# Performance work log

Measured on AMD Instinct MI355X. Metric: run time of the kernel, lower is better.

## Reference

```python
import jax, jax.numpy as jnp
import numpy as np
import math

D_IN, D_MODEL, N_HEADS, DIM_HEAD, NB_FEAT, N_CLASSES = 24, 512, 8, 64, 266, 10
FF_DIM = 4 * D_MODEL  # performer-pytorch FeedForward mult=4
LN_EPS = 1e-5
B, N = 16, 2048


def gaussian_orthogonal(key, nb_rows, nb_cols):
    # FAVOR+ gaussian orthogonal random matrix (scaling=0: chi-distributed row norms)
    n_blocks = nb_rows // nb_cols + 1
    keys = jax.random.split(key, n_blocks + 1)
    blocks = []
    for i in range(n_blocks):
        q, _ = jnp.linalg.qr(jax.random.normal(keys[i], (nb_cols, nb_cols)))
        blocks.append(q.T)
    mat = jnp.concatenate(blocks, axis=0)[:nb_rows]
    multiplier = jnp.linalg.norm(jax.random.normal(keys[-1], (nb_rows, nb_cols)), axis=1)
    return multiplier[:, None] * mat


def layer_norm(x, g, b):
    mu = jnp.mean(x, axis=-1, keepdims=True)
    var = jnp.var(x, axis=-1, keepdims=True)
    return (x - mu) * jax.lax.rsqrt(var + LN_EPS) * g + b


def softmax_kernel(data, proj, is_query, eps=1e-4):
    # FAVOR+ positive random features approximating the softmax kernel
    data_norm = data.shape[-1] ** -0.25
    ratio = proj.shape[0] ** -0.5
    dd = jnp.einsum('bhnd,fd->bhnf', data * data_norm, proj)  # [B,H,N,F]
    diag = 0.5 * jnp.sum(data * data, axis=-1, keepdims=True) * (data_norm ** 2)
    if is_query:
        m = jax.lax.stop_gradient(jnp.max(dd, axis=-1, keepdims=True))
    else:
        m = jax.lax.stop_gradient(jnp.max(dd))
    return ratio * (jnp.exp(dd - diag - m) + eps)


def setup_inputs() -> dict:
    key = jax.random.key(0)
    ks = jax.random.split(key, 24)

    def linw(k, fi, fo):
        bnd = 1.0 / math.sqrt(fi)
        return jax.random.uniform(k, (fi, fo), minval=-bnd, maxval=bnd, dtype=jnp.float32)

    def linb(k, fi, fo):
        bnd = 1.0 / math.sqrt(fi)
        return jax.random.uniform(k, (fo,), minval=-bnd, maxval=bnd, dtype=jnp.float32)

    return {
        'x': jax.random.normal(ks[0], (B, N, D_IN), dtype=jnp.float32),
        'enc_w': linw(ks[1], D_IN, D_MODEL), 'enc_b': linb(ks[2], D_IN, D_MODEL),
        'ln1_g': jnp.ones((D_MODEL,), jnp.float32), 'ln1_b': jnp.zeros((D_MODEL,), jnp.float32),
        'wq': linw(ks[3], D_MODEL, D_MODEL), 'bq': linb(ks[4], D_MODEL, D_MODEL),
        'wk': linw(ks[5], D_MODEL, D_MODEL), 'bk': linb(ks[6], D_MODEL, D_MODEL),
        'wv': linw(ks[7], D_MODEL, D_MODEL), 'bv': linb(ks[8], D_MODEL, D_MODEL),
        'wo': linw(ks[9], D_MODEL, D_MODEL), 'bo': linb(ks[10], D_MODEL, D_MODEL),
        'proj': gaussian_orthogonal(ks[11], NB_FEAT, DIM_HEAD).astype(jnp.float32),
        'ln2_g': jnp.ones((D_MODEL,), jnp.float32), 'ln2_b': jnp.zeros((D_MODEL,), jnp.float32),
        'ff_w1': linw(ks[12], D_MODEL, FF_DIM), 'ff_b1': linb(ks[13], D_MODEL, FF_DIM),
        'ff_w2': linw(ks[14], FF_DIM, D_MODEL), 'ff_b2': linb(ks[15], FF_DIM, D_MODEL),
        'mlp_w1': linw(ks[16], D_MODEL, D_MODEL), 'mlp_b1': linb(ks[17], D_MODEL, D_MODEL),
        'mlp_w2': linw(ks[18], D_MODEL, N_CLASSES), 'mlp_b2': linb(ks[19], D_MODEL, N_CLASSES),
    }


def reference(x, enc_w, enc_b, ln1_g, ln1_b, wq, bq, wk, bk, wv, bv, wo, bo, proj,
              ln2_g, ln2_b, ff_w1, ff_b1, ff_w2, ff_b2, mlp_w1, mlp_b1, mlp_w2, mlp_b2):
    b, n, _ = x.shape
    h = (x @ enc_w + enc_b) * math.sqrt(D_MODEL)  # [B,N,D]

    # --- Performer layer: PreLN + FAVOR+ self-attention ---
    y = layer_norm(h, ln1_g, ln1_b)
    split = lambda t: t.reshape(b, n, N_HEADS, DIM_HEAD).transpose(0, 2, 1, 3)  # [B,H,N,Dh]
    q = split(y @ wq + bq)
    k = split(y @ wk + bk)
    v = split(y @ wv + bv)
    qp = softmax_kernel(q, proj, is_query=True)   # [B,H,N,F]
    kp = softmax_kernel(k, proj, is_query=False)  # [B,H,N,F]
    # non-causal linear attention
    k_sum = kp.sum(axis=2)                                   # [B,H,F]
    d_inv = 1.0 / jnp.einsum('bhnf,bhf->bhn', qp, k_sum)     # [B,H,N]
    ctx = jnp.einsum('bhnf,bhnd->bhfd', kp, v)               # [B,H,F,Dh]
    attn = jnp.einsum('bhnf,bhfd,bhn->bhnd', qp, ctx, d_inv)
    attn = attn.transpose(0, 2, 1, 3).reshape(b, n, D_MODEL)
    h = h + attn @ wo + bo

    y = layer_norm(h, ln2_g, ln2_b)
    h = h + jax.nn.gelu(y @ ff_w1 + ff_b1, approximate=False) @ ff_w2 + ff_b2

    # --- max pool over sequence + MLP head ---
    p = jnp.max(h, axis=1)  # [B,D]
    return jax.nn.relu(p @ mlp_w1 + mlp_b1) @ mlp_w2 + mlp_b2  # [B,n_classes]
```

## Files before the change

### kernel.cpp

```cpp
#include <hip/hip_runtime.h>
#include <math.h>

typedef unsigned short u16;
typedef __bf16 bf16x8 __attribute__((ext_vector_type(8)));
typedef float f32x4 __attribute__((ext_vector_type(4)));
typedef u16 u16x8 __attribute__((ext_vector_type(8)));

#define DEVI static __device__ __forceinline__

#define NB 16
#define SEQ 2048
#define DM 512
#define DH 64
#define NF 266
#define NFP 288
#define FFD 2048
#define ROWS (NB*SEQ)
#define SQRT_DM 22.62741699796952f
#define DATA_NORM 0.3535533905932738f
#define RATIO 0.0613139073f
#define KEPS 1e-4f

DEVI u16 f2b(float f){
  union{float f; unsigned u;} c; c.f=f;
  unsigned r = c.u + 0x7FFFu + ((c.u>>16)&1u);
  return (u16)(r>>16);
}
DEVI float b2f(u16 v){
  union{unsigned u; float f;} c; c.u = ((unsigned)v)<<16; return c.f;
}
DEVI unsigned cvtpk(float a, float b){
  unsigned r;
  asm("v_cvt_pk_bf16_f32 %0, %1, %2" : "=v"(r) : "v"(a), "v"(b));
  return r;
}

DEVI f32x4 MFMA(bf16x8 a, bf16x8 b, f32x4 c){
  return __builtin_amdgcn_mfma_f32_16x16x32_bf16(a,b,c,0,0,0);
}

DEVI void async16(void* lds, const void* g){
  __builtin_amdgcn_global_load_lds(
      (const __attribute__((address_space(1))) unsigned*)g,
      (__attribute__((address_space(3))) unsigned*)lds, 16, 0, 0);
}

DEVI void atomicMaxF(float* a, float v){
  if (v >= 0.f) atomicMax((int*)a, __float_as_int(v));
  else          atomicMin((unsigned*)a, (unsigned)__float_as_int(v));
}

DEVI bf16x8 ldb8(const u16* p){ return *(const bf16x8*)p; }

DEVI float erf_fast(float u){
  float au = fabsf(u);
  float tt = __builtin_amdgcn_rcpf(1.f + 0.3275911f*au);
  float poly = tt*(0.254829592f + tt*(-0.284496736f + tt*(1.421413741f + tt*(-1.453152027f + tt*1.061405429f))));
  float er = 1.f - poly*__expf(-u*u);
  return copysignf(er, u);
}

template<int EPI>
__launch_bounds__(256,2)
__global__ void gemm_tn(const u16* __restrict__ A, int lda,
                        const u16* __restrict__ Bt, int ldb,
                        const float* __restrict__ bias,
                        float* __restrict__ resid,
                        u16* __restrict__ Cb,
                        int N, int K)
{
  __shared__ u16 As[2][128*32];
  __shared__ u16 Bs[2][128*32];
  const int t = threadIdx.x;
  const int ntn = N >> 7;
  int bid = blockIdx.x;
  const int nwg = gridDim.x;
  if ((nwg & 7) == 0){ int qq = nwg >> 3; bid = (bid & 7)*qq + (bid >> 3); }
  const int bm = bid / ntn, bn = bid % ntn;
  const int w = t>>6, l = t&63, lr = l&15, lg = l>>4;
  const int wr = (w>>1)*64, wc = (w&1)*64;
  const u16* ga = A  + (size_t)(bm*128 + (t>>2))*lda + (t&3)*8;
  const u16* gb = Bt + (size_t)(bn*128 + (t>>2))*ldb + (t&3)*8;
  const int nk = K >> 5;
  f32x4 acc[4][4];
  #pragma unroll
  for (int i=0;i<4;i++)
    #pragma unroll
    for (int j=0;j<4;j++) acc[i][j]=(f32x4){0.f,0.f,0.f,0.f};

  async16(&As[0][t*8], ga);
  async16(&As[0][64*32 + t*8], ga + (size_t)64*lda);
  async16(&Bs[0][t*8], gb);
  async16(&Bs[0][64*32 + t*8], gb + (size_t)64*ldb);

  for (int kt=0; kt<nk; ++kt){
    __syncthreads();
    if (kt+1 < nk){
      const u16* ga2 = ga + (kt+1)*32;
      const u16* gb2 = gb + (kt+1)*32;
      int nbuf = (kt+1)&1;
      async16(&As[nbuf][t*8], ga2);
      async16(&As[nbuf][64*32 + t*8], ga2 + (size_t)64*lda);
      async16(&Bs[nbuf][t*8], gb2);
      async16(&Bs[nbuf][64*32 + t*8], gb2 + (size_t)64*ldb);
    }
    const u16* as = As[kt&1];
    const u16* bs = Bs[kt&1];
    bf16x8 af[4], bff[4];
    #pragma unroll
    for (int i=0;i<4;i++) af[i]  = ldb8(&as[(wr + i*16 + lr)*32 + lg*8]);
    #pragma unroll
    for (int i=0;i<4;i++) bff[i] = ldb8(&bs[(wc + i*16 + lr)*32 + lg*8]);
    #pragma unroll
    for (int i=0;i<4;i++)
      #pragma unroll
      for (int j=0;j<4;j++)
        acc[i][j] = MFMA(af[i], bff[j], acc[i][j]);
  }

  const int r0 = bm*128 + wr + lg*4;
  const int c0 = bn*128 + wc + lr;
  #pragma unroll
  for (int i=0;i<4;i++){
    #pragma unroll
    for (int j=0;j<4;j++){
      #pragma unroll
      for (int q=0;q<4;q++){
        int r = r0 + i*16 + q;
        int c = c0 + j*16;
        float v = acc[i][j][q] + bias[c];
        if (EPI==2) v = 0.5f*v*(1.f + erf_fast(v*0.70710678f));
        size_t idx = (size_t)r*N + c;
        if (EPI==3) resid[idx] = resid[idx] + v;
        else        Cb[idx] = f2b(v);
      }
    }
  }
}

__launch_bounds__(256)
__global__ void k_prep(const float* __restrict__ wq, const float* __restrict__ wk,
                       const float* __restrict__ wv, const float* __restrict__ wo,
                       const float* __restrict__ ffw1, const float* __restrict__ ffw2,
                       const float* __restrict__ proj, const float* __restrict__ bk,
                       const float* __restrict__ bv,
                       u16* __restrict__ wqT, u16* __restrict__ wkvT, u16* __restrict__ woT,
                       u16* __restrict__ f1T, u16* __restrict__ f2T, u16* __restrict__ pjn,
                       float* __restrict__ kvb, float* __restrict__ pbuf)
{
  int bid = blockIdx.x, t = threadIdx.x;
  if (bid < 3072){
    const float* src; u16* dst; int R, C, tile;
    if      (bid < 256){ src=wq;  dst=wqT;          R=512; C=512;  tile=bid; }
    else if (bid < 512){ src=wk;  dst=wkvT;         R=512; C=512;  tile=bid-256; }
    else if (bid < 768){ src=wv;  dst=wkvT+262144;  R=512; C=512;  tile=bid-512; }
    else if (bid <1024){ src=wo;  dst=woT;          R=512; C=512;  tile=bid-768; }
    else if (bid <2048){ src=ffw1;dst=f1T;          R=512; C=2048; tile=bid-1024; }
    else               { src=ffw2;dst=f2T;          R=2048;C=512;  tile=bid-2048; }
    int ntc = C>>5;
    int tr = tile/ntc, tc = tile%ntc;
    __shared__ float tl[32][33];
    int r = t>>5, c = t&31;
    #pragma unroll
    for (int it=0; it<4; ++it)
      tl[r+it*8][c] = src[(size_t)(tr*32 + r + it*8)*C + tc*32 + c];
    __syncthreads();
    #pragma unroll
    for (int it=0; it<4; ++it)
      dst[(size_t)(tc*32 + r + it*8)*R + tr*32 + c] = f2b(tl[c][r+it*8]);
    return;
  }
  int i = (bid-3072)*256 + t;
  if (i < NFP*DH){ int f=i>>6, d=i&63; pjn[i] = f2b(f<NF ? proj[(size_t)f*64+d]*DATA_NORM : 0.f); return; }
  i -= NFP*DH;
  if (i < 1024){ kvb[i] = (i<512)? bk[i] : bv[i-512]; return; }
  i -= 1024;
  if (i < NB*DM){ pbuf[i] = -INFINITY; return; }
}

__global__ void k_signal(float* out, float v){
  if (threadIdx.x==0 && blockIdx.x==0) out[0] = v;
}

__launch_bounds__(256)
__global__ void k_encode_ln(const float* __restrict__ x, const float* __restrict__ ew,
                            const float* __restrict__ eb, const float* __restrict__ lgw,
                            const float* __restrict__ lbw, float* __restrict__ h,
                            u16* __restrict__ y)
{
  int w = threadIdx.x>>6, l = threadIdx.x&63;
  int row = blockIdx.x*4 + w;
  const float* xr = x + (size_t)row*24;
  float xv[24];
  #pragma unroll
  for (int k=0;k<24;k++) xv[k] = xr[k];
  int c0 = l*8;
  float a[8] = {0,0,0,0,0,0,0,0};
  #pragma unroll
  for (int k=0;k<24;k++){
    const float* wp = ew + (size_t)k*DM + c0;
    #pragma unroll
    for (int c=0;c<8;c++) a[c] += xv[k]*wp[c];
  }
  float s=0.f, s2=0.f;
  #pragma unroll
  for (int c=0;c<8;c++){
    a[c] = (a[c] + eb[c0+c]) * SQRT_DM;
    s += a[c]; s2 += a[c]*a[c];
  }
  #pragma unroll
  for (int m=1;m<64;m<<=1){ s += __shfl_xor(s,m); s2 += __shfl_xor(s2,m); }
  float mu = s*(1.f/DM);
  float rs = rsqrtf(s2*(1.f/DM) - mu*mu + 1e-5f);
  float* hr = h + (size_t)row*DM + c0;
  u16 yv[8];
  #pragma unroll
  for (int c=0;c<8;c++){
    hr[c] = a[c];
    yv[c] = f2b((a[c]-mu)*rs*lgw[c0+c] + lbw[c0+c]);
  }
  *(uint4*)(y + (size_t)row*DM + c0) = *(const uint4*)yv;
}

__launch_bounds__(256)
__global__ void k_ln(const float* __restrict__ h, const float* __restrict__ lgw,
                     const float* __restrict__ lbw, u16* __restrict__ y)
{
  int w = threadIdx.x>>6, l = threadIdx.x&63;
  int row = blockIdx.x*4 + w;
  int c0 = l*8;
  const float* hr = h + (size_t)row*DM + c0;
  float a[8];
  *(float4*)&a[0] = *(const float4*)hr;
  *(float4*)&a[4] = *(const float4*)(hr+4);
  float s=0.f, s2=0.f;
  #pragma unroll
  for (int c=0;c<8;c++){ s += a[c]; s2 += a[c]*a[c]; }
  #pragma unroll
  for (int m=1;m<64;m<<=1){ s += __shfl_xor(s,m); s2 += __shfl_xor(s2,m); }
  float mu = s*(1.f/DM);
  float rs = rsqrtf(s2*(1.f/DM) - mu*mu + 1e-5f);
  u16 yv[8];
  #pragma unroll
  for (int c=0;c<8;c++) yv[c] = f2b((a[c]-mu)*rs*lgw[c0+c] + lbw[c0+c]);
  *(uint4*)(y + (size_t)row*DM + c0) = *(const uint4*)yv;
}

__launch_bounds__(256,1)
__global__ void k_kmax(const u16* __restrict__ kv, const u16* __restrict__ pjn,
                       float* __restrict__ mkpart)
{
  __shared__ float red[4];
  int t = threadIdx.x, w = t>>6, l = t&63, lr = l&15, lg = l>>4;
  int bh = blockIdx.x>>3, tile = blockIdx.x&7;
  int b = bh>>3, hd = bh&7;
  int row0 = tile*256 + w*64;
  bf16x8 pf0[17], pf1[17];
  #pragma unroll
  for (int f=0; f<17; ++f){
    const u16* pb = pjn + (f*16 + lr)*64 + lg*8;
    pf0[f] = ldb8(pb); pf1[f] = ldb8(pb+32);
  }
  bf16x8 a0[4], a1[4];
  #pragma unroll
  for (int it=0; it<4; ++it){
    const u16* kb = kv + ((size_t)(b*SEQ + row0 + it*16 + lr)*1024 + hd*64 + lg*8);
    a0[it] = ldb8(kb); a1[it] = ldb8(kb+32);
  }
  float vmax = -3e38f;
  #pragma unroll
  for (int it=0; it<4; ++it){
    #pragma unroll
    for (int f=0; f<17; ++f){
      f32x4 z = (f32x4){0.f,0.f,0.f,0.f};
      z = MFMA(a0[it], pf0[f], z);
      z = MFMA(a1[it], pf1[f], z);
      if (f*16 + lr < NF){
        #pragma unroll
        for (int j=0;j<4;j++) vmax = fmaxf(vmax, z[j]);
      }
    }
  }
  #pragma unroll
  for (int m=1;m<64;m<<=1) vmax = fmaxf(vmax, __shfl_xor(vmax,m));
  if (l==0) red[w] = vmax;
  __syncthreads();
  if (t==0) mkpart[blockIdx.x] = fmaxf(fmaxf(red[0],red[1]), fmaxf(red[2],red[3]));
}

__global__ void k_kmax_red(const float* __restrict__ mkpart, float* __restrict__ mk){
  __shared__ float red[4];
  int t = threadIdx.x, w = t>>6, l = t&63;
  float v = fmaxf(fmaxf(mkpart[t], mkpart[t+256]), fmaxf(mkpart[t+512], mkpart[t+768]));
  #pragma unroll
  for (int m=1;m<64;m<<=1) v = fmaxf(v, __shfl_xor(v,m));
  if (l==0) red[w] = v;
  __syncthreads();
  if (t==0) mk[0] = fmaxf(fmaxf(red[0],red[1]), fmaxf(red[2],red[3]));
}

__launch_bounds__(256,2)
__global__ void k_kpctx(const u16* __restrict__ kv, const u16* __restrict__ pjn,
                        const float* __restrict__ mkp,
                        u16* __restrict__ ctxp, float* __restrict__ ksump)
{
  __shared__ u16 pjs[272*64];
  __shared__ u16 vT[DH*32];
  __shared__ u16 kpT[NFP*32];
  __shared__ float dbuf[4][16];
  int t = threadIdx.x, w = t>>6, l = t&63, lr = l&15, lg = l>>4;
  int bh = blockIdx.x>>2, seg = blockIdx.x&3;
  int b = bh>>3, hd = bh&7;
  int mw = w>>1, fh = (w&1)*9;
  float mk = *mkp;

  for (int i=t; i<2176; i+=256){
    int row = i>>3, cin = i&7;
    *(uint4*)&pjs[row*64 + ((cin ^ (row&7))<<3)] = ((const uint4*)pjn)[i];
  }

  f32x4 ctxa[18];
  #pragma unroll
  for (int f=0;f<18;f++) ctxa[f]=(f32x4){0.f,0.f,0.f,0.f};
  float ksa[9];
  #pragma unroll
  for (int i=0;i<9;i++) ksa[i]=0.f;

  for (int ch=0; ch<16; ++ch){
    int n0 = seg*512 + ch*32;
    __syncthreads();
    {
      int nl = t>>3, d0 = (t&7)*8;
      const u16* vsrc = kv + ((size_t)(b*SEQ + n0 + nl)*1024 + 512 + hd*64 + d0);
      uint4 vv = *(const uint4*)vsrc;
      const u16* vp = (const u16*)&vv;
      #pragma unroll
      for (int i=0;i<8;i++){
        int row = d0+i;
        vT[row*32 + (((nl>>3) ^ ((row>>1)&3))<<3) + (nl&7)] = vp[i];
      }
    }
    const u16* kb = kv + ((size_t)(b*SEQ + n0 + mw*16 + lr)*1024 + hd*64 + lg*8);
    bf16x8 a0 = ldb8(kb), a1 = ldb8(kb+32);
    float sq = 0.f;
    #pragma unroll
    for (int i=0;i<8;i++){ float u0=(float)a0[i], u1=(float)a1[i]; sq += u0*u0 + u1*u1; }
    sq += __shfl_xor(sq,16); sq += __shfl_xor(sq,32);
    if (l<16) dbuf[w][l] = sq*0.0625f;
    #pragma unroll
    for (int ff=0; ff<9; ++ff){
      int f = fh + ff;
      f32x4 z = (f32x4){0.f,0.f,0.f,0.f};
      if (f < 17){
        int row = f*16 + lr;
        const u16* pb0 = pjs + row*64 + ((lg ^ (lr&7))<<3);
        const u16* pb1 = pjs + row*64 + (((lg+4) ^ (lr&7))<<3);
        z = MFMA(a0, ldb8(pb0), z);
        z = MFMA(a1, ldb8(pb1), z);
      }
      float kp0 = RATIO*(__expf(z[0] - dbuf[w][lg*4+0] - mk) + KEPS);
      float kp1 = RATIO*(__expf(z[1] - dbuf[w][lg*4+1] - mk) + KEPS);
      float kp2 = RATIO*(__expf(z[2] - dbuf[w][lg*4+2] - mk) + KEPS);
      float kp3 = RATIO*(__expf(z[3] - dbuf[w][lg*4+3] - mk) + KEPS);
      ksa[ff] += kp0 + kp1 + kp2 + kp3;
      ushort4 kw;
      kw.x = f2b(kp0); kw.y = f2b(kp1); kw.z = f2b(kp2); kw.w = f2b(kp3);
      int row = f*16 + lr;
      int wch = (mw*2 + (lg>>1)) ^ ((row>>1)&3);
      *(ushort4*)&kpT[row*32 + (wch<<3) + ((lg&1)<<2)] = kw;
    }
    __syncthreads();
    int rr = w*16 + lr;
    bf16x8 av = ldb8(&vT[rr*32 + ((lg ^ ((rr>>1)&3))<<3)]);
    #pragma unroll
    for (int f=0;f<18;f++){
      int row = f*16 + lr;
      ctxa[f] = MFMA(av, ldb8(&kpT[row*32 + ((lg ^ ((row>>1)&3))<<3)]), ctxa[f]);
    }
  }

  __syncthreads();
  {
    float* tb = (w&1) ? (float*)pjs : (float*)kpT;
    u16* dstq = ctxp + (((size_t)seg*128 + bh)*DH + w*16)*NFP;
    #pragma unroll
    for (int r=0; r<2; ++r){
      if ((w>>1) == r){
        #pragma unroll
        for (int f=0;f<18;f++)
          #pragma unroll
          for (int j=0;j<4;j++)
            tb[(lg*4+j)*NFP + f*16 + lr] = ctxa[f][j];
        asm volatile("s_waitcnt lgkmcnt(0)" ::: "memory");
        #pragma unroll
        for (int k=0;k<9;k++){
          int c = k*64 + l;
          f32x4 v0 = *(const f32x4*)(tb + c*8);
          f32x4 v1 = *(const f32x4*)(tb + c*8 + 4);
          u16x8 o;
          o[0]=f2b(v0[0]); o[1]=f2b(v0[1]); o[2]=f2b(v0[2]); o[3]=f2b(v0[3]);
          o[4]=f2b(v1[0]); o[5]=f2b(v1[1]); o[6]=f2b(v1[2]); o[7]=f2b(v1[3]);
          *(u16x8*)(dstq + c*8) = o;
        }
      }
      __syncthreads();
    }
  }
  #pragma unroll
  for (int ff=0;ff<9;ff++){
    float v = ksa[ff];
    v += __shfl_xor(v,16); v += __shfl_xor(v,32);
    if (l<16) ksump[((size_t)seg*128 + bh)*NFP + (fh+ff)*16 + l] = v;
  }
}

__global__ void k_reduce(const u16* __restrict__ ctxp, const float* __restrict__ ksump,
                         u16* __restrict__ ctxb, float* __restrict__ ksum)
{
  const size_t CT = (size_t)128*DH*NFP;
  const size_t KT = (size_t)128*NFP;
  size_t i = (size_t)blockIdx.x*256 + threadIdx.x;
  if (i < CT){
    float s = b2f(ctxp[i]) + b2f(ctxp[i+CT]) + b2f(ctxp[i+2*CT]) + b2f(ctxp[i+3*CT]);
    ctxb[i] = f2b(s);
  } else if (i < CT + KT){
    size_t j = i - CT;
    ksum[j] = ksump[j] + ksump[j+KT] + ksump[j+2*KT] + ksump[j+3*KT];
  }
}

__launch_bounds__(256,3)
__global__ void k_qp_attn(const u16* __restrict__ q, const u16* __restrict__ pjn,
                          const u16* __restrict__ ctxb, const float* __restrict__ ksum,
                          u16* __restrict__ attn)
{
  __shared__ u16 ob[4][16*72];
  int t = threadIdx.x, w = t>>6, l = t&63, lr = l&15, lg = l>>4;
  int bh = blockIdx.x>>5, tile = blockIdx.x&31;
  int b = bh>>3, hd = bh&7;
  int n0 = tile*64;
  const u16* qb = q + ((size_t)(b*SEQ + n0 + w*16 + lr)*DM + hd*64 + lg*8);
  bf16x8 a0 = ldb8(qb), a1 = ldb8(qb+32);
  float sq = 0.f;
  #pragma unroll
  for (int i=0;i<8;i++){ float u0=(float)a0[i], u1=(float)a1[i]; sq += u0*u0 + u1*u1; }
  sq += __shfl_xor(sq,16); sq += __shfl_xor(sq,32);
  float dg = sq*0.0625f;

  float mj = -3e38f;
  #pragma unroll
  for (int ft=0; ft<17; ++ft){
    const u16* pb = pjn + (ft*16 + lr)*64 + lg*8;
    f32x4 z = (f32x4){0.f,0.f,0.f,0.f};
    z = MFMA(ldb8(pb), a0, z);
    z = MFMA(ldb8(pb+32), a1, z);
    if (ft < 16){
      #pragma unroll
      for (int j=0;j<4;j++) mj = fmaxf(mj, z[j]);
    } else {
      #pragma unroll
      for (int j=0;j<4;j++) if (lg*4+j < 10) mj = fmaxf(mj, z[j]);
    }
  }
  mj = fmaxf(mj, __shfl_xor(mj,16));
  mj = fmaxf(mj, __shfl_xor(mj,32));

  int s0 = ((lg&1)<<5) + lr;
  int s1 = s0 + 16;
  bool hi = (l >= 32);
  f32x4 oacc[4];
  #pragma unroll
  for (int d=0;d<4;d++) oacc[d]=(f32x4){0.f,0.f,0.f,0.f};
  const u16* cbase = ctxb + (size_t)bh*DH*NFP;
  const float* ksb = ksum + (size_t)bh*NFP;
  float den = 0.f;
  #pragma unroll
  for (int fp=0; fp<9; ++fp){
    int te = 2*fp, to = te+1;
    f32x4 z0 = (f32x4){0.f,0.f,0.f,0.f};
    f32x4 z1 = (f32x4){0.f,0.f,0.f,0.f};
    {
      const u16* pb = pjn + (te*16 + lr)*64 + lg*8;
      z0 = MFMA(ldb8(pb), a0, z0);
      z0 = MFMA(ldb8(pb+32), a1, z0);
    }
    if (to < 17){
      const u16* pb = pjn + (to*16 + lr)*64 + lg*8;
      z1 = MFMA(ldb8(pb), a0, z1);
      z1 = MFMA(ldb8(pb+32), a1, z1);
    }
    f32x4 ks0 = *(const f32x4*)(ksb + te*16 + lg*4);
    f32x4 ks1 = *(const f32x4*)(ksb + to*16 + lg*4);
    int fb0 = te*16 + lg*4, fb1 = to*16 + lg*4;
    float qv0[4], qv1[4];
    #pragma unroll
    for (int j=0;j<4;j++){
      qv0[j] = (fb0 + j < NF) ? RATIO*(__expf(z0[j] - dg - mj) + KEPS) : 0.f;
      den += qv0[j]*ks0[j];
      qv1[j] = (fb1 + j < NF) ? RATIO*(__expf(z1[j] - dg - mj) + KEPS) : 0.f;
      den += qv1[j]*ks1[j];
    }
    unsigned q00 = cvtpk(qv0[0], qv0[1]), q01 = cvtpk(qv0[2], qv0[3]);
    unsigned q10 = cvtpk(qv1[0], qv1[1]), q11 = cvtpk(qv1[2], qv1[3]);
    unsigned e0 = (unsigned)__shfl((int)q00, s0), o0 = (unsigned)__shfl((int)q10, s0);
    unsigned e1 = (unsigned)__shfl((int)q01, s0), o1 = (unsigned)__shfl((int)q11, s0);
    unsigned e2 = (unsigned)__shfl((int)q00, s1), o2 = (unsigned)__shfl((int)q10, s1);
    unsigned e3 = (unsigned)__shfl((int)q01, s1), o3 = (unsigned)__shfl((int)q11, s1);
    union { unsigned u[4]; bf16x8 v; } bw;
    bw.u[0] = hi ? o0 : e0;
    bw.u[1] = hi ? o1 : e1;
    bw.u[2] = hi ? o2 : e2;
    bw.u[3] = hi ? o3 : e3;
    #pragma unroll
    for (int d=0;d<4;d++)
      oacc[d] = MFMA(bw.v, ldb8(&cbase[(d*16 + lr)*NFP + fp*32 + lg*8]), oacc[d]);
  }
  den += __shfl_xor(den,16); den += __shfl_xor(den,32);
  float di = 1.f/den;
  float di4[4];
  #pragma unroll
  for (int j=0;j<4;j++) di4[j] = __shfl(di, lg*4+j);

  u16* obw = ob[w];
  #pragma unroll
  for (int d=0;d<4;d++)
    #pragma unroll
    for (int j=0;j<4;j++)
      obw[(lg*4+j)*72 + d*16 + lr] = f2b(oacc[d][j]*di4[j]);
  asm volatile("s_waitcnt lgkmcnt(0)" ::: "memory");
  {
    int row = l>>2, ck = l&3;
    uint4 v0 = *(const uint4*)&obw[row*72 + ck*8];
    uint4 v1 = *(const uint4*)&obw[row*72 + (ck+4)*8];
    u16* ab = attn + ((size_t)(b*SEQ + n0 + w*16 + row))*DM + hd*64;
    *(uint4*)(ab + ck*8) = v0;
    *(uint4*)(ab + (ck+4)*8) = v1;
  }
}

__global__ void k_maxpool(const float* __restrict__ h, float* __restrict__ p){
  int bi = blockIdx.x;
  int b = bi>>5, half = (bi>>4)&1, seg = bi&15;
  int c = half*256 + threadIdx.x;
  const float* hp = h + ((size_t)b*SEQ + seg*128)*DM + c;
  float m = -3e38f;
  for (int n=0;n<128;n++) m = fmaxf(m, hp[(size_t)n*DM]);
  atomicMaxF(&p[b*DM + c], m);
}

__launch_bounds__(256)
__global__ void k_head(const float* __restrict__ p, const float* __restrict__ w1,
                       const float* __restrict__ b1, const float* __restrict__ w2,
                       const float* __restrict__ b2, float* __restrict__ out)
{
  __shared__ float z[DM];
  __shared__ float pr[DM];
  int b = blockIdx.x, t = threadIdx.x;
  pr[t] = p[(size_t)b*DM + t];
  pr[t+256] = p[(size_t)b*DM + t + 256];
  __syncthreads();
  for (int c=t; c<DM; c+=256){
    float a = b1[c];
    for (int k=0;k<DM;k++) a += pr[k]*w1[(size_t)k*DM + c];
    z[c] = fmaxf(a, 0.f);
  }
  __syncthreads();
  if (t < 10){
    float a = b2[t];
    for (int k=0;k<DM;k++) a += z[k]*w2[(size_t)k*10 + t];
    out[b*10 + t] = a;
  }
}

static inline size_t align256(size_t x){ return (x+255)&~(size_t)255; }

extern "C" void kernel_launch(void* const* d_in, const int* in_sizes, int n_in,
                              void* d_out, int out_size, void* d_ws, size_t ws_size,
                              hipStream_t stream)
{
  (void)in_sizes; (void)n_in; (void)out_size;
  const float* x     = (const float*)d_in[0];
  const float* enc_w = (const float*)d_in[1];
  const float* enc_b = (const float*)d_in[2];
  const float* ln1_g = (const float*)d_in[3];
  const float* ln1_b = (const float*)d_in[4];
  const float* wq    = (const float*)d_in[5];
  const float* bq    = (const float*)d_in[6];
  const float* wk    = (const float*)d_in[7];
  const float* bk    = (const float*)d_in[8];
  const float* wv    = (const float*)d_in[9];
  const float* bv    = (const float*)d_in[10];
  const float* wo    = (const float*)d_in[11];
  const float* bo    = (const float*)d_in[12];
  const float* proj  = (const float*)d_in[13];
  const float* ln2_g = (const float*)d_in[14];
  const float* ln2_b = (const float*)d_in[15];
  const float* ff_w1 = (const float*)d_in[16];
  const float* ff_b1 = (const float*)d_in[17];
  const float* ff_w2 = (const float*)d_in[18];
  const float* ff_b2 = (const float*)d_in[19];
  const float* mw1   = (const float*)d_in[20];
  const float* mb1   = (const float*)d_in[21];
  const float* mw2   = (const float*)d_in[22];
  const float* mb2   = (const float*)d_in[23];

  char* base = (char*)d_ws;
  size_t off = 0;
  auto alloc = [&](size_t bytes)->void*{ void* r = base + off; off = align256(off + bytes); return r; };
  float* h     = (float*)alloc((size_t)ROWS*DM*4);
  u16*   slotA = (u16*)  alloc((size_t)ROWS*DM*2);
  u16*   slotB = (u16*)  alloc((size_t)ROWS*1024*2);
  u16*   wqT   = (u16*)  alloc((size_t)512*512*2);
  u16*   wkvT  = (u16*)  alloc((size_t)1024*512*2);
  u16*   woT   = (u16*)  alloc((size_t)512*512*2);
  u16*   f1T   = (u16*)  alloc((size_t)2048*512*2);
  u16*   f2T   = (u16*)  alloc((size_t)512*2048*2);
  u16*   pjn   = (u16*)  alloc((size_t)NFP*DH*2);
  float* kvb   = (float*)alloc(1024*4);
  float* mk    = (float*)alloc(256);
  float* mkpart= (float*)alloc(1024*4);
  u16*   ctxp  = (u16*)  alloc((size_t)4*128*DH*NFP*2);
  float* ksump = (float*)alloc((size_t)4*128*NFP*4);
  u16*   ctxb  = (u16*)  alloc((size_t)128*DH*NFP*2);
  float* ksum  = (float*)alloc((size_t)128*NFP*4);
  float* pbuf  = (float*)alloc((size_t)NB*DM*4);

  if (off > ws_size){
    k_signal<<<1,64,0,stream>>>((float*)d_out, (float)ws_size);
    return;
  }

  u16* y    = slotA;
  u16* attn = slotA;
  u16* kvB  = slotB;
  u16* qB   = slotB;
  u16* ffb  = slotB;

  k_prep<<<3180,256,0,stream>>>(wq, wk, wv, wo, ff_w1, ff_w2, proj, bk, bv,
                                wqT, wkvT, woT, f1T, f2T, pjn, kvb, pbuf);

  k_encode_ln<<<ROWS/4,256,0,stream>>>(x, enc_w, enc_b, ln1_g, ln1_b, h, y);
  gemm_tn<1><<<(ROWS/128)*(1024/128),256,0,stream>>>(y,512, wkvT,512, kvb, nullptr, kvB, 1024, 512);
  k_kmax<<<1024,256,0,stream>>>(kvB, pjn, mkpart);
  k_kmax_red<<<1,256,0,stream>>>(mkpart, mk);
  k_kpctx<<<512,256,0,stream>>>(kvB, pjn, mk, ctxp, ksump);
  k_reduce<<<9360,256,0,stream>>>(ctxp, ksump, ctxb, ksum);
  gemm_tn<1><<<(ROWS/128)*(512/128),256,0,stream>>>(y,512, wqT,512, bq, nullptr, qB, 512, 512);
  k_qp_attn<<<128*32,256,0,stream>>>(qB, pjn, ctxb, ksum, attn);
  gemm_tn<3><<<(ROWS/128)*(512/128),256,0,stream>>>(attn,512, woT,512, bo, h, nullptr, 512, 512);
  k_ln<<<ROWS/4,256,0,stream>>>(h, ln2_g, ln2_b, y);
  for (int c2=0;c2<2;c2++){
    const u16* ych = y + (size_t)c2*16384*512;
    float*     hch = h + (size_t)c2*16384*512;
    gemm_tn<2><<<(16384/128)*(2048/128),256,0,stream>>>(ych,512, f1T,512, ff_b1, nullptr, ffb, 2048, 512);
    gemm_tn<3><<<(16384/128)*(512/128),256,0,stream>>>(ffb,2048, f2T,2048, ff_b2, hch, nullptr, 512, 2048);
  }
  k_maxpool<<<NB*32,256,0,stream>>>(h, pbuf);
  k_head<<<NB,256,0,stream>>>(pbuf, mw1, mb1, mw2, mb2, (float*)d_out);
}
```

Before: 708.0 us.

## Replace GEMM with 256x256-tile 8-wave triple-buffered swizzled kernel and merge FFN chunks

Replaces the 128x128 double-buffered GEMM with a 512-thread kernel that computes 256x256 tiles, uses a three-stage async LDS pipeline with XOR-swizzled layout and raises wave priority around the MFMA block. This aims to raise data reuse per loaded tile, hide global-load latency and cut LDS bank conflicts. When the workspace is large enough, the FFN runs as a single pass over all rows instead of two chunks, which needs a larger intermediate buffer. The attention output store is also reshaped so each lane writes one contiguous 16-byte piece per row. The large tile uses many accumulator registers, which risks spills or lower occupancy.

```diff
diff --git a/kernel.cpp b/kernel.cpp
--- a/kernel.cpp
+++ b/kernel.cpp
@@ -61,74 +61,101 @@
 }
 
 template<int EPI>
-__launch_bounds__(256,2)
-__global__ void gemm_tn(const u16* __restrict__ A, int lda,
-                        const u16* __restrict__ Bt, int ldb,
-                        const float* __restrict__ bias,
-                        float* __restrict__ resid,
-                        u16* __restrict__ Cb,
-                        int N, int K)
-{
-  __shared__ u16 As[2][128*32];
-  __shared__ u16 Bs[2][128*32];
-  const int t = threadIdx.x;
-  const int ntn = N >> 7;
+__launch_bounds__(512,2)
+__global__ void gemm8(const u16* __restrict__ A, int lda,
+                      const u16* __restrict__ Bt, int ldb,
+                      const float* __restrict__ bias,
+                      float* __restrict__ resid,
+                      u16* __restrict__ Cb,
+                      int N, int K)
+{
+  __shared__ u16 sm[49152];
+  const int tid = threadIdx.x;
+  const int ntn = N >> 8;
   int bid = blockIdx.x;
   const int nwg = gridDim.x;
   if ((nwg & 7) == 0){ int qq = nwg >> 3; bid = (bid & 7)*qq + (bid >> 3); }
   const int bm = bid / ntn, bn = bid % ntn;
-  const int w = t>>6, l = t&63, lr = l&15, lg = l>>4;
-  const int wr = (w>>1)*64, wc = (w&1)*64;
-  const u16* ga = A  + (size_t)(bm*128 + (t>>2))*lda + (t&3)*8;
-  const u16* gb = Bt + (size_t)(bn*128 + (t>>2))*ldb + (t&3)*8;
-  const int nk = K >> 5;
-  f32x4 acc[4][4];
-  #pragma unroll
-  for (int i=0;i<4;i++)
-    #pragma unroll
-    for (int j=0;j<4;j++) acc[i][j]=(f32x4){0.f,0.f,0.f,0.f};
-
-  async16(&As[0][t*8], ga);
-  async16(&As[0][64*32 + t*8], ga + (size_t)64*lda);
-  async16(&Bs[0][t*8], gb);
-  async16(&Bs[0][64*32 + t*8], gb + (size_t)64*ldb);
-
-  for (int kt=0; kt<nk; ++kt){
-    __syncthreads();
-    if (kt+1 < nk){
-      const u16* ga2 = ga + (kt+1)*32;
-      const u16* gb2 = gb + (kt+1)*32;
-      int nbuf = (kt+1)&1;
-      async16(&As[nbuf][t*8], ga2);
-      async16(&As[nbuf][64*32 + t*8], ga2 + (size_t)64*lda);
-      async16(&Bs[nbuf][t*8], gb2);
-      async16(&Bs[nbuf][64*32 + t*8], gb2 + (size_t)64*ldb);
-    }
-    const u16* as = As[kt&1];
-    const u16* bs = Bs[kt&1];
-    bf16x8 af[4], bff[4];
-    #pragma unroll
-    for (int i=0;i<4;i++) af[i]  = ldb8(&as[(wr + i*16 + lr)*32 + lg*8]);
-    #pragma unroll
-    for (int i=0;i<4;i++) bff[i] = ldb8(&bs[(wc + i*16 + lr)*32 + lg*8]);
-    #pragma unroll
-    for (int i=0;i<4;i++)
+  const int wid = tid>>6, l = tid&63, lr = l&15, lg = l>>4;
+  const int wm = wid>>2, wn = wid&3;
+
+  const int rA = tid>>2;
+  const int cA = (tid&3) ^ ((rA>>1)&3);
+  const u16* gA = A  + (size_t)(bm*256 + rA)*lda + cA*8;
+  const u16* gB = Bt + (size_t)(bn*256 + rA)*ldb + cA*8;
+  const size_t stepA = (size_t)128*lda, stepB = (size_t)128*ldb;
+
+  const int cc = ((lg ^ ((lr>>1)&3))<<3);
+  const int aoff = (wm*128 + lr)*32 + cc;
+  const int boff = 8192 + (wn*64 + lr)*32 + cc;
+
+  const int nt = K >> 5;
+  f32x4 acc[8][4];
+  #pragma unroll
+  for (int m=0;m<8;m++)
+    #pragma unroll
+    for (int n=0;n<4;n++) acc[m][n]=(f32x4){0.f,0.f,0.f,0.f};
+
+  #pragma unroll
+  for (int p=0;p<2;p++){
+    u16* sb = &sm[p*16384];
+    const u16* a0 = gA + p*32;
+    const u16* b0 = gB + p*32;
+    async16(&sb[tid*8],         a0);
+    async16(&sb[4096 + tid*8],  a0 + stepA);
+    async16(&sb[8192 + tid*8],  b0);
+    async16(&sb[12288 + tid*8], b0 + stepB);
+  }
+  asm volatile("s_waitcnt vmcnt(4)" ::: "memory");
+  __builtin_amdgcn_s_barrier();
+  __builtin_amdgcn_sched_barrier(0);
+
+  int bcur = 0;
+  for (int t=0; t<nt; ++t){
+    if (t+2 < nt){
+      int btg = bcur+2; if (btg>=3) btg-=3;
+      u16* sb = &sm[btg*16384];
+      const u16* a0 = gA + (t+2)*32;
+      const u16* b0 = gB + (t+2)*32;
+      async16(&sb[tid*8],         a0);
+      async16(&sb[4096 + tid*8],  a0 + stepA);
+      async16(&sb[8192 + tid*8],  b0);
+      async16(&sb[12288 + tid*8], b0 + stepB);
+    }
+    __builtin_amdgcn_sched_barrier(0);
+    const u16* sb = &sm[bcur*16384];
+    bf16x8 af[8], bfr[4];
+    #pragma unroll
+    for (int m=0;m<8;m++) af[m]  = ldb8(&sb[aoff + m*512]);
+    #pragma unroll
+    for (int n=0;n<4;n++) bfr[n] = ldb8(&sb[boff + n*512]);
+    __builtin_amdgcn_s_setprio(1);
+    #pragma unroll
+    for (int m=0;m<8;m++)
       #pragma unroll
-      for (int j=0;j<4;j++)
-        acc[i][j] = MFMA(af[i], bff[j], acc[i][j]);
-  }
-
-  const int r0 = bm*128 + wr + lg*4;
-  const int c0 = bn*128 + wc + lr;
-  #pragma unroll
-  for (int i=0;i<4;i++){
-    #pragma unroll
-    for (int j=0;j<4;j++){
+      for (int n=0;n<4;n++)
+        acc[m][n] = MFMA(af[m], bfr[n], acc[m][n]);
+    __builtin_amdgcn_s_setprio(0);
+    if (t+1 < nt){
+      if (t+2 < nt) asm volatile("s_waitcnt vmcnt(4)" ::: "memory");
+      else          asm volatile("s_waitcnt vmcnt(0)" ::: "memory");
+      __builtin_amdgcn_s_barrier();
+      __builtin_amdgcn_sched_barrier(0);
+    }
+    bcur = (bcur==2) ? 0 : bcur+1;
+  }
+
+  const int r0 = bm*256 + wm*128 + lg*4;
+  const int c0 = bn*256 + wn*64 + lr;
+  #pragma unroll
+  for (int m=0;m<8;m++){
+    #pragma unroll
+    for (int n=0;n<4;n++){
       #pragma unroll
       for (int q=0;q<4;q++){
-        int r = r0 + i*16 + q;
-        int c = c0 + j*16;
-        float v = acc[i][j][q] + bias[c];
+        int r = r0 + m*16 + q;
+        int c = c0 + n*16;
+        float v = acc[m][n][q] + bias[c];
         if (EPI==2) v = 0.5f*v*(1.f + erf_fast(v*0.70710678f));
         size_t idx = (size_t)r*N + c;
         if (EPI==3) resid[idx] = resid[idx] + v;
@@ -529,12 +556,14 @@
       obw[(lg*4+j)*72 + d*16 + lr] = f2b(oacc[d][j]*di4[j]);
   asm volatile("s_waitcnt lgkmcnt(0)" ::: "memory");
   {
-    int row = l>>2, ck = l&3;
-    uint4 v0 = *(const uint4*)&obw[row*72 + ck*8];
-    uint4 v1 = *(const uint4*)&obw[row*72 + (ck+4)*8];
-    u16* ab = attn + ((size_t)(b*SEQ + n0 + w*16 + row))*DM + hd*64;
-    *(uint4*)(ab + ck*8) = v0;
-    *(uint4*)(ab + (ck+4)*8) = v1;
+    int row = l>>3, ck = l&7;
+    #pragma unroll
+    for (int rr=0; rr<2; ++rr){
+      int r2 = row + rr*8;
+      uint4 v = *(const uint4*)&obw[r2*72 + ck*8];
+      u16* ab = attn + ((size_t)(b*SEQ + n0 + w*16 + r2))*DM + hd*64;
+      *(uint4*)(ab + ck*8) = v;
+    }
   }
 }
 
@@ -609,7 +638,6 @@
   auto alloc = [&](size_t bytes)->void*{ void* r = base + off; off = align256(off + bytes); return r; };
   float* h     = (float*)alloc((size_t)ROWS*DM*4);
   u16*   slotA = (u16*)  alloc((size_t)ROWS*DM*2);
-  u16*   slotB = (u16*)  alloc((size_t)ROWS*1024*2);
   u16*   wqT   = (u16*)  alloc((size_t)512*512*2);
   u16*   wkvT  = (u16*)  alloc((size_t)1024*512*2);
   u16*   woT   = (u16*)  alloc((size_t)512*512*2);
@@ -619,13 +647,18 @@
   float* kvb   = (float*)alloc(1024*4);
   float* mk    = (float*)alloc(256);
   float* mkpart= (float*)alloc(1024*4);
-  u16*   ctxp  = (u16*)  alloc((size_t)4*128*DH*NFP*2);
-  float* ksump = (float*)alloc((size_t)4*128*NFP*4);
   u16*   ctxb  = (u16*)  alloc((size_t)128*DH*NFP*2);
   float* ksum  = (float*)alloc((size_t)128*NFP*4);
   float* pbuf  = (float*)alloc((size_t)NB*DM*4);
-
-  if (off > ws_size){
+  size_t offU = off;
+  u16*   slotB = (u16*)  alloc((size_t)ROWS*1024*2);
+  u16*   ctxp  = (u16*)  alloc((size_t)4*128*DH*NFP*2);
+  float* ksump = (float*)alloc((size_t)4*128*NFP*4);
+  size_t off_small = off;
+  size_t off_big   = align256(offU + (size_t)ROWS*FFD*2);
+  bool big = (off_big <= ws_size);
+  u16* ffb = (u16*)(base + offU);
+  if (off_small > ws_size){
     k_signal<<<1,64,0,stream>>>((float*)d_out, (float)ws_size);
     return;
   }
@@ -634,26 +667,30 @@
   u16* attn = slotA;
   u16* kvB  = slotB;
   u16* qB   = slotB;
-  u16* ffb  = slotB;
 
   k_prep<<<3180,256,0,stream>>>(wq, wk, wv, wo, ff_w1, ff_w2, proj, bk, bv,
                                 wqT, wkvT, woT, f1T, f2T, pjn, kvb, pbuf);
 
   k_encode_ln<<<ROWS/4,256,0,stream>>>(x, enc_w, enc_b, ln1_g, ln1_b, h, y);
-  gemm_tn<1><<<(ROWS/128)*(1024/128),256,0,stream>>>(y,512, wkvT,512, kvb, nullptr, kvB, 1024, 512);
+  gemm8<1><<<(ROWS/256)*(1024/256),512,0,stream>>>(y,512, wkvT,512, kvb, nullptr, kvB, 1024, 512);
   k_kmax<<<1024,256,0,stream>>>(kvB, pjn, mkpart);
   k_kmax_red<<<1,256,0,stream>>>(mkpart, mk);
   k_kpctx<<<512,256,0,stream>>>(kvB, pjn, mk, ctxp, ksump);
   k_reduce<<<9360,256,0,stream>>>(ctxp, ksump, ctxb, ksum);
-  gemm_tn<1><<<(ROWS/128)*(512/128),256,0,stream>>>(y,512, wqT,512, bq, nullptr, qB, 512, 512);
+  gemm8<1><<<(ROWS/256)*(512/256),512,0,stream>>>(y,512, wqT,512, bq, nullptr, qB, 512, 512);
   k_qp_attn<<<128*32,256,0,stream>>>(qB, pjn, ctxb, ksum, attn);
-  gemm_tn<3><<<(ROWS/128)*(512/128),256,0,stream>>>(attn,512, woT,512, bo, h, nullptr, 512, 512);
+  gemm8<3><<<(ROWS/256)*(512/256),512,0,stream>>>(attn,512, woT,512, bo, h, nullptr, 512, 512);
   k_ln<<<ROWS/4,256,0,stream>>>(h, ln2_g, ln2_b, y);
-  for (int c2=0;c2<2;c2++){
-    const u16* ych = y + (size_t)c2*16384*512;
-    float*     hch = h + (size_t)c2*16384*512;
-    gemm_tn<2><<<(16384/128)*(2048/128),256,0,stream>>>(ych,512, f1T,512, ff_b1, nullptr, ffb, 2048, 512);
-    gemm_tn<3><<<(16384/128)*(512/128),256,0,stream>>>(ffb,2048, f2T,2048, ff_b2, hch, nullptr, 512, 2048);
+  if (big){
+    gemm8<2><<<(ROWS/256)*(2048/256),512,0,stream>>>(y,512, f1T,512, ff_b1, nullptr, ffb, 2048, 512);
+    gemm8<3><<<(ROWS/256)*(512/256),512,0,stream>>>(ffb,2048, f2T,2048, ff_b2, h, nullptr, 512, 2048);
+  } else {
+    for (int c2=0;c2<2;c2++){
+      const u16* ych = y + (size_t)c2*16384*512;
+      float*     hch = h + (size_t)c2*16384*512;
+      gemm8<2><<<(16384/256)*(2048/256),512,0,stream>>>(ych,512, f1T,512, ff_b1, nullptr, ffb, 2048, 512);
+      gemm8<3><<<(16384/256)*(512/256),512,0,stream>>>(ffb,2048, f2T,2048, ff_b2, hch, nullptr, 512, 2048);
+    }
   }
   k_maxpool<<<NB*32,256,0,stream>>>(h, pbuf);
   k_head<<<NB,256,0,stream>>>(pbuf, mw1, mb1, mw2, mb2, (float*)d_out);
```

Measured after the change: 699.1 us. Within noise of the previous version (-1.3%).
